# Performance work log

Measured on AMD Instinct MI355X. Metric: run time of the kernel, lower is better.

## Reference

```python
import jax, jax.numpy as jnp
import numpy as np

U = 128  # linear_units

def setup_inputs() -> dict:
    key = jax.random.key(0)
    k1, k2, k3, k4, k5, k6 = jax.random.split(key, 6)
    B, S, D = 16, 2048, 128
    x = jax.random.normal(k1, (B, S, D), dtype=jnp.float32)
    t = jax.random.uniform(k2, (B, S), dtype=jnp.float32)
    # glorot_uniform inits
    lim_qk = np.sqrt(6.0 / (D + U)).astype(np.float32)
    Wq = jax.random.uniform(k3, (D, U), minval=-lim_qk, maxval=lim_qk, dtype=jnp.float32)
    Wk = jax.random.uniform(k4, (D, U), minval=-lim_qk, maxval=lim_qk, dtype=jnp.float32)
    lim_s = np.sqrt(6.0 / (1 + S)).astype(np.float32)
    theta = jax.random.uniform(k5, (1, S), minval=-lim_s, maxval=lim_s, dtype=jnp.float32)
    mu = jax.random.uniform(k6, (1, S), minval=-lim_s, maxval=lim_s, dtype=jnp.float32)
    return {"x": x, "t": t, "Wq": Wq, "Wk": Wk, "theta": theta, "mu": mu}

def reference(x, t, Wq, Wk, theta, mu):
    # x: (B,S,D), t: (B,S), theta/mu: (1,S)
    scale = jnp.sqrt(jnp.asarray(U, dtype=x.dtype))
    q = x @ Wq                                   # (B,S,U)
    k = x @ Wk                                   # (B,S,U)
    scores = jnp.einsum('biu,bju->bij', q, k) / scale  # (B,S,S)
    alphas = jax.nn.softmax(scores, axis=-1)
    gn = jnp.einsum('bij,bjd->bid', alphas, x)   # weighted sum == alphas @ x, (B,S,D)
    time_fact = jax.nn.sigmoid(theta - mu * t)   # (B,S)
    v = jnp.sum(gn * time_fact[:, :, None], axis=1)  # (B,D)
    return v
```

## Files before the change

kernel.cpp:

```cpp
#include <hip/hip_runtime.h>
#include <hip/hip_bf16.h>

#define SS 2048
#define DD 128
#define BB 16
#define LDST 136
#define SCT 268

typedef short bf16x8 __attribute__((ext_vector_type(8)));
typedef float f32x4 __attribute__((ext_vector_type(4)));
typedef unsigned short ushort_t;

__device__ __forceinline__ unsigned short f2bf(float f) {
  union { float f; unsigned u; } v; v.f = f;
  unsigned r = v.u + 0x7fffu + ((v.u >> 16) & 1u);
  return (unsigned short)(r >> 16);
}
__device__ __forceinline__ float fexp2(float x) { return __builtin_amdgcn_exp2f(x); }


__global__ __launch_bounds__(256) void wprep(
    const float* __restrict__ Wq, const float* __restrict__ Wk,
    ushort_t* __restrict__ wt_g) {
  int idx = blockIdx.x * 256 + threadIdx.x;
  int r = idx & 16383, uu = r >> 7, d = r & 127;
  if (idx < 16384)
    wt_g[uu * 128 + d] = f2bf(Wq[d * 128 + uu] * 0.1275174346f);
  else
    wt_g[(uu + 128) * 128 + d] = f2bf(Wk[d * 128 + uu]);
}

__global__ __launch_bounds__(256, 2) void qk_gemm(
    const float* __restrict__ x, const ushort_t* __restrict__ wt_g,
    uint4* __restrict__ qF, uint4* __restrict__ kF) {
  __shared__ ushort_t xs[64 * LDST];
  __shared__ ushort_t sc[64 * SCT];
  const int tid = threadIdx.x, wave = tid >> 6, lane = tid & 63;
  const int lq = lane & 15, quad = lane >> 4;
  const int m0 = blockIdx.x * 64;

#pragma unroll
  for (int i = 0; i < 8; ++i) {
    int idx = i * 256 + tid;
    int row = idx >> 5, c4 = (idx & 31) * 4;
    const float4 v = *(const float4*)(x + (size_t)(m0 + row) * DD + c4);
    ushort4 h;
    h.x = f2bf(v.x); h.y = f2bf(v.y); h.z = f2bf(v.z); h.w = f2bf(v.w);
    *(ushort4*)(&xs[row * LDST + c4]) = h;
  }
  bf16x8 wf[4][4];
#pragma unroll
  for (int nt = 0; nt < 4; ++nt)
#pragma unroll
    for (int ks = 0; ks < 4; ++ks)
      wf[nt][ks] = *(const bf16x8*)(wt_g + (wave * 64 + nt * 16 + lq) * 128 + ks * 32 + quad * 8);
  __syncthreads();

  f32x4 acc[4][4];
#pragma unroll
  for (int mt = 0; mt < 4; ++mt)
#pragma unroll
    for (int nt = 0; nt < 4; ++nt) acc[mt][nt] = (f32x4){0.f, 0.f, 0.f, 0.f};
#pragma unroll
  for (int mt = 0; mt < 4; ++mt) {
    bf16x8 af[4];
#pragma unroll
    for (int ks = 0; ks < 4; ++ks)
      af[ks] = *(const bf16x8*)(&xs[(mt * 16 + lq) * LDST + ks * 32 + quad * 8]);
#pragma unroll
    for (int nt = 0; nt < 4; ++nt)
#pragma unroll
      for (int ks = 0; ks < 4; ++ks)
        acc[mt][nt] = __builtin_amdgcn_mfma_f32_16x16x32_bf16(af[ks], wf[nt][ks], acc[mt][nt], 0, 0, 0);
  }
#pragma unroll
  for (int mt = 0; mt < 4; ++mt)
#pragma unroll
    for (int nt = 0; nt < 4; ++nt)
#pragma unroll
      for (int r = 0; r < 4; ++r)
        sc[(mt * 16 + quad * 4 + r) * SCT + wave * 64 + nt * 16 + lq] = f2bf(acc[mt][nt][r]);
  __syncthreads();
#pragma unroll
  for (int i = 0; i < 8; ++i) {
    int c = i * 256 + tid;
    int lane_c = c & 63, ks_c = (c >> 6) & 3, g_c = (c >> 8) & 3, isk = c >> 10;
    int li = lane_c & 15, qd = lane_c >> 4;
    int col = isk * 128 + ks_c * 32 + qd * 8;
    uint4 v = *(const uint4*)(&sc[(g_c * 16 + li) * SCT + col]);
    size_t G = (size_t)blockIdx.x * 4 + g_c;
    uint4* dst = isk ? kF : qF;
    dst[(G * 4 + ks_c) * 64 + lane_c] = v;
  }
}

__global__ __launch_bounds__(256, 4) void pass1(
    const uint4* __restrict__ qF, const uint4* __restrict__ kF,
    float* __restrict__ l) {
  const int blk = blockIdx.x;
  const int jc = blk & 1, ib = (blk >> 1) & 31, b = blk >> 6;
  const int i0 = ib * 64;
  const int tid = threadIdx.x, wave = tid >> 6, lane = tid & 63;
  const int quad = lane >> 4;

  const bf16x8* qc = (const bf16x8*)qF;
  const bf16x8* kc = (const bf16x8*)kF;

  bf16x8 af[4][4];
#pragma unroll
  for (int mt = 0; mt < 4; ++mt)
#pragma unroll
    for (int ks = 0; ks < 4; ++ks)
      af[mt][ks] = qc[((size_t)(b * 128 + ib * 4 + mt) * 4 + ks) * 64 + lane];

  float rowsum[4][4];
#pragma unroll
  for (int mt = 0; mt < 4; ++mt)
#pragma unroll
    for (int r = 0; r < 4; ++r) rowsum[mt][r] = 0.f;

  for (int s = 0; s < 16; ++s) {
    const int gg = b * 128 + jc * 64 + s * 4 + wave;
    bf16x8 bf[4];
#pragma unroll
    for (int ks = 0; ks < 4; ++ks)
      bf[ks] = kc[((size_t)gg * 4 + ks) * 64 + lane];
    f32x4 acc[4];
#pragma unroll
    for (int mt = 0; mt < 4; ++mt) acc[mt] = (f32x4){0.f, 0.f, 0.f, 0.f};
#pragma unroll
    for (int ks = 0; ks < 4; ++ks)
#pragma unroll
      for (int mt = 0; mt < 4; ++mt)
        acc[mt] = __builtin_amdgcn_mfma_f32_16x16x32_bf16(af[mt][ks], bf[ks], acc[mt], 0, 0, 0);
#pragma unroll
    for (int mt = 0; mt < 4; ++mt)
#pragma unroll
      for (int r = 0; r < 4; ++r) rowsum[mt][r] += fexp2(acc[mt][r]);
  }
#pragma unroll
  for (int d2 = 1; d2 <= 8; d2 <<= 1)
#pragma unroll
    for (int mt = 0; mt < 4; ++mt)
#pragma unroll
      for (int r = 0; r < 4; ++r)
        rowsum[mt][r] += __shfl_xor(rowsum[mt][r], d2, 64);
  if ((lane & 15) == 0) {
#pragma unroll
    for (int mt = 0; mt < 4; ++mt)
#pragma unroll
      for (int r = 0; r < 4; ++r)
        atomicAdd(&l[b * SS + i0 + mt * 16 + quad * 4 + r], rowsum[mt][r]);
  }
}

__global__ __launch_bounds__(256) void cvec(
    const float* __restrict__ t, const float* __restrict__ theta,
    const float* __restrict__ mu, const float* __restrict__ l,
    float* __restrict__ c) {
  int idx = blockIdx.x * 256 + threadIdx.x;
  int i = idx & 2047;
  float z = theta[i] - mu[i] * t[idx];
  float tf = 1.f / (1.f + fexp2(-z * 1.44269504f));
  c[idx] = tf / l[idx];
}

__global__ __launch_bounds__(256, 4) void pass2(
    const uint4* __restrict__ qF, const uint4* __restrict__ kF,
    const float* __restrict__ c, float* __restrict__ w) {
  const int blk = blockIdx.x;
  const int jc = blk & 1, ib = (blk >> 1) & 31, b = blk >> 6;
  const int i0 = ib * 64;
  const int tid = threadIdx.x, wave = tid >> 6, lane = tid & 63;
  const int quad = lane >> 4;

  const bf16x8* qc = (const bf16x8*)qF;
  const bf16x8* kc = (const bf16x8*)kF;

  bf16x8 af[4][4];
#pragma unroll
  for (int mt = 0; mt < 4; ++mt)
#pragma unroll
    for (int ks = 0; ks < 4; ++ks)
      af[mt][ks] = qc[((size_t)(b * 128 + ib * 4 + mt) * 4 + ks) * 64 + lane];

  float creg[4][4];
#pragma unroll
  for (int mt = 0; mt < 4; ++mt)
#pragma unroll
    for (int r = 0; r < 4; ++r)
      creg[mt][r] = c[b * SS + i0 + mt * 16 + quad * 4 + r];

  for (int s = 0; s < 16; ++s) {
    const int ggl = jc * 64 + s * 4 + wave;
    const int gg = b * 128 + ggl;
    bf16x8 bf[4];
#pragma unroll
    for (int ks = 0; ks < 4; ++ks)
      bf[ks] = kc[((size_t)gg * 4 + ks) * 64 + lane];
    f32x4 acc[4];
#pragma unroll
    for (int mt = 0; mt < 4; ++mt) acc[mt] = (f32x4){0.f, 0.f, 0.f, 0.f};
#pragma unroll
    for (int ks = 0; ks < 4; ++ks)
#pragma unroll
      for (int mt = 0; mt < 4; ++mt)
        acc[mt] = __builtin_amdgcn_mfma_f32_16x16x32_bf16(af[mt][ks], bf[ks], acc[mt], 0, 0, 0);
    float cs = 0.f;
#pragma unroll
    for (int mt = 0; mt < 4; ++mt)
#pragma unroll
      for (int r = 0; r < 4; ++r) cs = fmaf(creg[mt][r], fexp2(acc[mt][r]), cs);
    cs += __shfl_xor(cs, 16, 64);
    cs += __shfl_xor(cs, 32, 64);
    if (lane < 16)
      atomicAdd(&w[b * SS + ggl * 16 + lane], cs);
  }
}

__global__ __launch_bounds__(256) void finalize(
    const float* __restrict__ x, const float* __restrict__ w,
    float* __restrict__ out) {
  const int b = blockIdx.x >> 5;
  const int j0 = (blockIdx.x & 31) * 64;
  const int tid = threadIdx.x;
  const int d = tid & 127, jo = tid >> 7;
  float acc = 0.f;
  for (int jj = 0; jj < 32; ++jj) {
    int j = j0 + jj * 2 + jo;
    acc = fmaf(w[b * SS + j], x[((size_t)b * SS + j) * DD + d], acc);
  }
  __shared__ float red[256];
  red[tid] = acc;
  __syncthreads();
  if (tid < 128) atomicAdd(&out[b * DD + tid], red[tid] + red[tid + 128]);
}

extern "C" void kernel_launch(void* const* d_in, const int* in_sizes, int n_in,
                              void* d_out, int out_size, void* d_ws, size_t ws_size,
                              hipStream_t stream) {
  const float* x = (const float*)d_in[0];
  const float* t = (const float*)d_in[1];
  const float* Wq = (const float*)d_in[2];
  const float* Wk = (const float*)d_in[3];
  const float* theta = (const float*)d_in[4];
  const float* mu = (const float*)d_in[5];
  float* out = (float*)d_out;

  uint4* qF = (uint4*)d_ws;
  uint4* kF = qF + (size_t)2048 * 4 * 64;
  ushort_t* wt_g = (ushort_t*)(kF + (size_t)2048 * 4 * 64);
  float* l = (float*)(wt_g + 256 * 128);
  float* c = l + (size_t)BB * SS;
  float* w = c + (size_t)BB * SS;

  hipMemsetAsync(l, 0, (size_t)BB * SS * sizeof(float), stream);
  hipMemsetAsync(w, 0, (size_t)BB * SS * sizeof(float), stream);
  hipMemsetAsync(d_out, 0, (size_t)BB * DD * sizeof(float), stream);

  wprep<<<dim3(128), dim3(256), 0, stream>>>(Wq, Wk, wt_g);
  qk_gemm<<<dim3(512), dim3(256), 0, stream>>>(x, wt_g, qF, kF);
  pass1<<<dim3(1024), dim3(256), 0, stream>>>(qF, kF, l);
  cvec<<<dim3(128), dim3(256), 0, stream>>>(t, theta, mu, l, c);
  pass2<<<dim3(1024), dim3(256), 0, stream>>>(qF, kF, c, w);
  finalize<<<dim3(512), dim3(256), 0, stream>>>(x, w, out);
}
```

Measured before the change: 137.1 us.

## Stage K tiles through LDS with async double buffering and retile passes

```diff
diff --git a/kernel.cpp b/kernel.cpp
--- a/kernel.cpp
+++ b/kernel.cpp
@@ -5,7 +5,6 @@
 #define DD 128
 #define BB 16
 #define LDST 136
-#define SCT 268
 
 typedef short bf16x8 __attribute__((ext_vector_type(8)));
 typedef float f32x4 __attribute__((ext_vector_type(4)));
@@ -17,6 +16,12 @@
   return (unsigned short)(r >> 16);
 }
 __device__ __forceinline__ float fexp2(float x) { return __builtin_amdgcn_exp2f(x); }
+
+typedef const __attribute__((address_space(1))) unsigned int* gas_t;
+typedef __attribute__((address_space(3))) unsigned int* las_t;
+__device__ __forceinline__ void async16(const void* g, void* l) {
+  __builtin_amdgcn_global_load_lds((gas_t)g, (las_t)l, 16, 0, 0);
+}
 
 
 __global__ __launch_bounds__(256) void wprep(
@@ -30,14 +35,15 @@
     wt_g[(uu + 128) * 128 + d] = f2bf(Wk[d * 128 + uu]);
 }
 
-__global__ __launch_bounds__(256, 2) void qk_gemm(
+__global__ __launch_bounds__(256, 4) void qk_gemm(
     const float* __restrict__ x, const ushort_t* __restrict__ wt_g,
     uint4* __restrict__ qF, uint4* __restrict__ kF) {
   __shared__ ushort_t xs[64 * LDST];
-  __shared__ ushort_t sc[64 * SCT];
+  __shared__ ushort_t sc[64 * LDST];
   const int tid = threadIdx.x, wave = tid >> 6, lane = tid & 63;
   const int lq = lane & 15, quad = lane >> 4;
-  const int m0 = blockIdx.x * 64;
+  const int rt = blockIdx.x >> 1, isk = blockIdx.x & 1;
+  const int m0 = rt * 64;
 
 #pragma unroll
   for (int i = 0; i < 8; ++i) {
@@ -48,19 +54,19 @@
     h.x = f2bf(v.x); h.y = f2bf(v.y); h.z = f2bf(v.z); h.w = f2bf(v.w);
     *(ushort4*)(&xs[row * LDST + c4]) = h;
   }
-  bf16x8 wf[4][4];
-#pragma unroll
-  for (int nt = 0; nt < 4; ++nt)
-#pragma unroll
-    for (int ks = 0; ks < 4; ++ks)
-      wf[nt][ks] = *(const bf16x8*)(wt_g + (wave * 64 + nt * 16 + lq) * 128 + ks * 32 + quad * 8);
-  __syncthreads();
-
-  f32x4 acc[4][4];
-#pragma unroll
-  for (int mt = 0; mt < 4; ++mt)
-#pragma unroll
-    for (int nt = 0; nt < 4; ++nt) acc[mt][nt] = (f32x4){0.f, 0.f, 0.f, 0.f};
+  bf16x8 wf[2][4];
+#pragma unroll
+  for (int nt = 0; nt < 2; ++nt)
+#pragma unroll
+    for (int ks = 0; ks < 4; ++ks)
+      wf[nt][ks] = *(const bf16x8*)(wt_g + (isk * 128 + wave * 32 + nt * 16 + lq) * 128 + ks * 32 + quad * 8);
+  __syncthreads();
+
+  f32x4 acc[4][2];
+#pragma unroll
+  for (int mt = 0; mt < 4; ++mt)
+#pragma unroll
+    for (int nt = 0; nt < 2; ++nt) acc[mt][nt] = (f32x4){0.f, 0.f, 0.f, 0.f};
 #pragma unroll
   for (int mt = 0; mt < 4; ++mt) {
     bf16x8 af[4];
@@ -68,7 +74,7 @@
     for (int ks = 0; ks < 4; ++ks)
       af[ks] = *(const bf16x8*)(&xs[(mt * 16 + lq) * LDST + ks * 32 + quad * 8]);
 #pragma unroll
-    for (int nt = 0; nt < 4; ++nt)
+    for (int nt = 0; nt < 2; ++nt)
 #pragma unroll
       for (int ks = 0; ks < 4; ++ks)
         acc[mt][nt] = __builtin_amdgcn_mfma_f32_16x16x32_bf16(af[ks], wf[nt][ks], acc[mt][nt], 0, 0, 0);
@@ -76,20 +82,19 @@
 #pragma unroll
   for (int mt = 0; mt < 4; ++mt)
 #pragma unroll
-    for (int nt = 0; nt < 4; ++nt)
+    for (int nt = 0; nt < 2; ++nt)
 #pragma unroll
       for (int r = 0; r < 4; ++r)
-        sc[(mt * 16 + quad * 4 + r) * SCT + wave * 64 + nt * 16 + lq] = f2bf(acc[mt][nt][r]);
-  __syncthreads();
-#pragma unroll
-  for (int i = 0; i < 8; ++i) {
+        sc[(mt * 16 + quad * 4 + r) * LDST + wave * 32 + nt * 16 + lq] = f2bf(acc[mt][nt][r]);
+  __syncthreads();
+  uint4* dst = isk ? kF : qF;
+#pragma unroll
+  for (int i = 0; i < 4; ++i) {
     int c = i * 256 + tid;
-    int lane_c = c & 63, ks_c = (c >> 6) & 3, g_c = (c >> 8) & 3, isk = c >> 10;
+    int lane_c = c & 63, ks_c = (c >> 6) & 3, g_c = c >> 8;
     int li = lane_c & 15, qd = lane_c >> 4;
-    int col = isk * 128 + ks_c * 32 + qd * 8;
-    uint4 v = *(const uint4*)(&sc[(g_c * 16 + li) * SCT + col]);
-    size_t G = (size_t)blockIdx.x * 4 + g_c;
-    uint4* dst = isk ? kF : qF;
+    uint4 v = *(const uint4*)(&sc[(g_c * 16 + li) * LDST + ks_c * 32 + qd * 8]);
+    size_t G = (size_t)rt * 4 + g_c;
     dst[(G * 4 + ks_c) * 64 + lane_c] = v;
   }
 }
@@ -97,21 +102,25 @@
 __global__ __launch_bounds__(256, 4) void pass1(
     const uint4* __restrict__ qF, const uint4* __restrict__ kF,
     float* __restrict__ l) {
+  __shared__ alignas(16) unsigned char kbuf[2][4096];
   const int blk = blockIdx.x;
-  const int jc = blk & 1, ib = (blk >> 1) & 31, b = blk >> 6;
-  const int i0 = ib * 64;
+  const int jc = blk & 7, ib = (blk >> 3) & 7, b = blk >> 6;
   const int tid = threadIdx.x, wave = tid >> 6, lane = tid & 63;
   const int quad = lane >> 4;
 
   const bf16x8* qc = (const bf16x8*)qF;
-  const bf16x8* kc = (const bf16x8*)kF;
-
   bf16x8 af[4][4];
 #pragma unroll
   for (int mt = 0; mt < 4; ++mt)
 #pragma unroll
     for (int ks = 0; ks < 4; ++ks)
-      af[mt][ks] = qc[((size_t)(b * 128 + ib * 4 + mt) * 4 + ks) * 64 + lane];
+      af[mt][ks] = qc[((size_t)(b * 128 + ib * 16 + wave * 4 + mt) * 4 + ks) * 64 + lane];
+
+  const unsigned char* kbase =
+      (const unsigned char*)kF + ((size_t)(b * 128 + jc * 16)) * 4096;
+  auto stage = [&](int s, int buf) {
+    async16(kbase + (size_t)s * 4096 + tid * 16, &kbuf[buf][wave * 1024]);
+  };
 
   float rowsum[4][4];
 #pragma unroll
@@ -119,12 +128,14 @@
 #pragma unroll
     for (int r = 0; r < 4; ++r) rowsum[mt][r] = 0.f;
 
+  stage(0, 0);
+  __syncthreads();
   for (int s = 0; s < 16; ++s) {
-    const int gg = b * 128 + jc * 64 + s * 4 + wave;
+    if (s + 1 < 16) stage(s + 1, (s + 1) & 1);
+    const bf16x8* kb = (const bf16x8*)(&kbuf[s & 1][0]);
     bf16x8 bf[4];
 #pragma unroll
-    for (int ks = 0; ks < 4; ++ks)
-      bf[ks] = kc[((size_t)gg * 4 + ks) * 64 + lane];
+    for (int ks = 0; ks < 4; ++ks) bf[ks] = kb[ks * 64 + lane];
     f32x4 acc[4];
 #pragma unroll
     for (int mt = 0; mt < 4; ++mt) acc[mt] = (f32x4){0.f, 0.f, 0.f, 0.f};
@@ -137,6 +148,7 @@
     for (int mt = 0; mt < 4; ++mt)
 #pragma unroll
       for (int r = 0; r < 4; ++r) rowsum[mt][r] += fexp2(acc[mt][r]);
+    __syncthreads();
   }
 #pragma unroll
   for (int d2 = 1; d2 <= 8; d2 <<= 1)
@@ -150,54 +162,55 @@
     for (int mt = 0; mt < 4; ++mt)
 #pragma unroll
       for (int r = 0; r < 4; ++r)
-        atomicAdd(&l[b * SS + i0 + mt * 16 + quad * 4 + r], rowsum[mt][r]);
-  }
-}
-
-__global__ __launch_bounds__(256) void cvec(
+        atomicAdd(&l[b * SS + ib * 256 + wave * 64 + mt * 16 + quad * 4 + r],
+                  rowsum[mt][r]);
+  }
+}
+
+__global__ __launch_bounds__(256, 4) void pass2(
+    const uint4* __restrict__ qF, const uint4* __restrict__ kF,
     const float* __restrict__ t, const float* __restrict__ theta,
     const float* __restrict__ mu, const float* __restrict__ l,
-    float* __restrict__ c) {
-  int idx = blockIdx.x * 256 + threadIdx.x;
-  int i = idx & 2047;
-  float z = theta[i] - mu[i] * t[idx];
-  float tf = 1.f / (1.f + fexp2(-z * 1.44269504f));
-  c[idx] = tf / l[idx];
-}
-
-__global__ __launch_bounds__(256, 4) void pass2(
-    const uint4* __restrict__ qF, const uint4* __restrict__ kF,
-    const float* __restrict__ c, float* __restrict__ w) {
+    float* __restrict__ w) {
+  __shared__ alignas(16) unsigned char kbuf[2][4096];
   const int blk = blockIdx.x;
-  const int jc = blk & 1, ib = (blk >> 1) & 31, b = blk >> 6;
-  const int i0 = ib * 64;
+  const int jc = blk & 7, ib = (blk >> 3) & 7, b = blk >> 6;
   const int tid = threadIdx.x, wave = tid >> 6, lane = tid & 63;
   const int quad = lane >> 4;
 
   const bf16x8* qc = (const bf16x8*)qF;
-  const bf16x8* kc = (const bf16x8*)kF;
-
   bf16x8 af[4][4];
 #pragma unroll
   for (int mt = 0; mt < 4; ++mt)
 #pragma unroll
     for (int ks = 0; ks < 4; ++ks)
-      af[mt][ks] = qc[((size_t)(b * 128 + ib * 4 + mt) * 4 + ks) * 64 + lane];
+      af[mt][ks] = qc[((size_t)(b * 128 + ib * 16 + wave * 4 + mt) * 4 + ks) * 64 + lane];
 
   float creg[4][4];
 #pragma unroll
   for (int mt = 0; mt < 4; ++mt)
 #pragma unroll
-    for (int r = 0; r < 4; ++r)
-      creg[mt][r] = c[b * SS + i0 + mt * 16 + quad * 4 + r];
-
+    for (int r = 0; r < 4; ++r) {
+      int gi = ib * 256 + wave * 64 + mt * 16 + quad * 4 + r;
+      float z = theta[gi] - mu[gi] * t[b * SS + gi];
+      float tf = 1.f / (1.f + fexp2(-z * 1.44269504f));
+      creg[mt][r] = tf / l[b * SS + gi];
+    }
+
+  const unsigned char* kbase =
+      (const unsigned char*)kF + ((size_t)(b * 128 + jc * 16)) * 4096;
+  auto stage = [&](int s, int buf) {
+    async16(kbase + (size_t)s * 4096 + tid * 16, &kbuf[buf][wave * 1024]);
+  };
+
+  stage(0, 0);
+  __syncthreads();
   for (int s = 0; s < 16; ++s) {
-    const int ggl = jc * 64 + s * 4 + wave;
-    const int gg = b * 128 + ggl;
+    if (s + 1 < 16) stage(s + 1, (s + 1) & 1);
+    const bf16x8* kb = (const bf16x8*)(&kbuf[s & 1][0]);
     bf16x8 bf[4];
 #pragma unroll
-    for (int ks = 0; ks < 4; ++ks)
-      bf[ks] = kc[((size_t)gg * 4 + ks) * 64 + lane];
+    for (int ks = 0; ks < 4; ++ks) bf[ks] = kb[ks * 64 + lane];
     f32x4 acc[4];
 #pragma unroll
     for (int mt = 0; mt < 4; ++mt) acc[mt] = (f32x4){0.f, 0.f, 0.f, 0.f};
@@ -214,7 +227,8 @@
     cs += __shfl_xor(cs, 16, 64);
     cs += __shfl_xor(cs, 32, 64);
     if (lane < 16)
-      atomicAdd(&w[b * SS + ggl * 16 + lane], cs);
+      atomicAdd(&w[b * SS + (jc * 16 + s) * 16 + lane], cs);
+    __syncthreads();
   }
 }
 
@@ -251,17 +265,14 @@
   uint4* kF = qF + (size_t)2048 * 4 * 64;
   ushort_t* wt_g = (ushort_t*)(kF + (size_t)2048 * 4 * 64);
   float* l = (float*)(wt_g + 256 * 128);
-  float* c = l + (size_t)BB * SS;
-  float* w = c + (size_t)BB * SS;
-
-  hipMemsetAsync(l, 0, (size_t)BB * SS * sizeof(float), stream);
-  hipMemsetAsync(w, 0, (size_t)BB * SS * sizeof(float), stream);
+  float* w = l + (size_t)BB * SS;
+
+  hipMemsetAsync(l, 0, (size_t)2 * BB * SS * sizeof(float), stream);
   hipMemsetAsync(d_out, 0, (size_t)BB * DD * sizeof(float), stream);
 
   wprep<<<dim3(128), dim3(256), 0, stream>>>(Wq, Wk, wt_g);
-  qk_gemm<<<dim3(512), dim3(256), 0, stream>>>(x, wt_g, qF, kF);
+  qk_gemm<<<dim3(1024), dim3(256), 0, stream>>>(x, wt_g, qF, kF);
   pass1<<<dim3(1024), dim3(256), 0, stream>>>(qF, kF, l);
-  cvec<<<dim3(128), dim3(256), 0, stream>>>(t, theta, mu, l, c);
-  pass2<<<dim3(1024), dim3(256), 0, stream>>>(qF, kF, c, w);
+  pass2<<<dim3(1024), dim3(256), 0, stream>>>(qF, kF, t, theta, mu, l, w);
   finalize<<<dim3(512), dim3(256), 0, stream>>>(x, w, out);
 }
```

Result: slower. 143.0 us (+4.3%).
